# Optimization experiments

Measured on AMD Instinct MI355X. Metric: run time of the kernel, lower is better.

## Reference

```python
import jax, jax.numpy as jnp
import numpy as np

KS = 3            # kernel_size
DILS = (1, 2, 4)  # dilation_list == padding_list
EPS = 1e-5        # BN eps


def _unfold3(x, d):
    # emulate F.unfold(kernel=3, dilation=d, padding=d, stride=1).view(b, c, 9, h, w)
    b, c, h, w = x.shape
    xp = jnp.pad(x, ((0, 0), (0, 0), (d, d), (d, d)))
    pats = [xp[:, :, i * d:i * d + h, j * d:j * d + w] for i in range(KS) for j in range(KS)]
    return jnp.stack(pats, axis=2)


def _conv1x1(x, w, b):
    return jnp.einsum('bchw,oc->bohw', x, w) + b[None, :, None, None]


def _bn_relu(x, g, be, m, v):
    s = g / jnp.sqrt(v + EPS)
    return jax.nn.relu(x * s[None, :, None, None] + (be - m * s)[None, :, None, None])


def _proj(x, w1, b1, g1, be1, m1, v1, w2, b2, g2, be2, m2, v2):
    h = _bn_relu(_conv1x1(x, w1, b1), g1, be1, m1, v1)
    return _bn_relu(_conv1x1(h, w2, b2), g2, be2, m2, v2)


def setup_inputs():
    key = jax.random.key(0)
    Cin, Ck, Cv, Cout = 512, 256, 256, 512
    B, H, W = 4, 64, 64
    ks = iter(jax.random.split(key, 48))

    def nrm(shape, s=0.02):
        return jax.random.normal(next(ks), shape, jnp.float32) * s

    def bn(c):
        return (jnp.ones((c,), jnp.float32) + nrm((c,), 0.1),  # gamma
                nrm((c,), 0.1),                                 # beta
                nrm((c,), 0.1),                                 # running mean
                jax.random.uniform(next(ks), (c,), jnp.float32, 0.5, 1.5))  # running var

    inp = {"x": jax.random.normal(next(ks), (B, Cin, H, W), jnp.float32)}
    for p in ("k", "q"):
        g1, be1, m1, v1 = bn(Ck)
        g2, be2, m2, v2 = bn(Ck)
        inp.update({
            p + "1_w": nrm((Ck, Cin)), p + "1_b": nrm((Ck,)),
            p + "1_g": g1, p + "1_be": be1, p + "1_m": m1, p + "1_v": v1,
            p + "2_w": nrm((Ck, Ck)), p + "2_b": nrm((Ck,)),
            p + "2_g": g2, p + "2_be": be2, p + "2_m": m2, p + "2_v": v2,
        })
    inp["v_w"] = nrm((Cv, Cin)); inp["v_b"] = nrm((Cv,))
    inp["w_w"] = nrm((Cout, Cv)); inp["w_b"] = nrm((Cout,))
    return inp


def reference(x,
              k1_w, k1_b, k1_g, k1_be, k1_m, k1_v,
              k2_w, k2_b, k2_g, k2_be, k2_m, k2_v,
              q1_w, q1_b, q1_g, q1_be, q1_m, q1_v,
              q2_w, q2_b, q2_g, q2_be, q2_m, q2_v,
              v_w, v_b, w_w, w_b):
    # scale == 1: MaxPool2d(1x1-equivalent) and final bilinear resize are identities.
    value = _conv1x1(x, v_w, v_b)                                  # (b,cv,h,w)
    keyf = _proj(x, k1_w, k1_b, k1_g, k1_be, k1_m, k1_v,
                 k2_w, k2_b, k2_g, k2_be, k2_m, k2_v)              # (b,ck,h,w)
    query = _proj(x, q1_w, q1_b, q1_g, q1_be, q1_m, q1_v,
                  q2_w, q2_b, q2_g, q2_be, q2_m, q2_v)             # (b,ck,h,w)
    uk = jnp.concatenate([_unfold3(keyf, d) for d in DILS], axis=2)   # (b,ck,27,h,w)
    uv = jnp.concatenate([_unfold3(value, d) for d in DILS], axis=2)  # (b,cv,27,h,w)
    sim = jnp.sum(uk * query[:, :, None], axis=1, keepdims=True)      # (b,1,27,h,w)
    sim = jax.nn.softmax(sim, axis=2)
    context = jnp.sum(sim * uv, axis=2)                               # (b,cv,h,w)
    return _conv1x1(context, w_w, w_b)
```

## Files before the change

### kernel.cpp

```cpp
#include <hip/hip_runtime.h>

#define HW   4096
#define Hh   64
#define Ww   64
#define NB   27
#define EPSBN 1e-5f

typedef _Float16 f16x8 __attribute__((ext_vector_type(8)));
typedef _Float16 f16x4 __attribute__((ext_vector_type(4)));
typedef _Float16 f16x2 __attribute__((ext_vector_type(2)));
typedef float    f32x4 __attribute__((ext_vector_type(4)));

__device__ __forceinline__ void gld_lds16(const void* g, void* l) {
    __builtin_amdgcn_global_load_lds(
        (const __attribute__((address_space(1))) unsigned int*)g,
        (__attribute__((address_space(3))) unsigned int*)l, 16, 0, 0);
}

__global__ __launch_bounds__(256)
void prep_kernel(const float* s0, const float* s1, const float* s2,
                 const float* s3, const float* s4, const float* s5,
                 _Float16* d0, _Float16* d1, _Float16* d2,
                 _Float16* d3, _Float16* d4, _Float16* d5)
{
    const int bid = blockIdx.x;
    const int j  = bid >> 6;
    const int bx = bid & 63;
    const float* s = j==0?s0: j==1?s1: j==2?s2: j==3?s3: j==4?s4: s5;
    _Float16*  d = j==0?d0: j==1?d1: j==2?d2: j==3?d3: j==4?d4: d5;
    const int  n = (j==3 || j==4) ? 65536 : 131072;
    const int  i = (bx * 256 + threadIdx.x) * 8;
    if (i < n) {
        f16x8 h;
        #pragma unroll
        for (int k = 0; k < 8; ++k) h[k] = (_Float16)s[i + k];
        *(f16x8*)(d + i) = h;
    }
}

struct GJob {
    const _Float16* in;
    const float*    xf;
    const _Float16* w;
    const float* b; const float* g; const float* be; const float* m; const float* v;
    _Float16* oh;
    float*    of;
};

__global__ __launch_bounds__(512)
void gemm_f(GJob J0, GJob J1, GJob J2, int stage, int K, int JO, int mode)
{
    __shared__ _Float16 As[3 * 64 * 64];
    __shared__ _Float16 Bs[128 * 64];

    const int tid  = threadIdx.x;
    const int lane = tid & 63;
    const int w8   = tid >> 6;
    const int lr   = lane & 15;
    const int lg   = lane >> 4;
    const int wm   = w8 & 3;
    const int wn   = w8 >> 2;

    const int bid = blockIdx.x;
    const int xcd = bid & 7;
    const int jj  = bid >> 3;
    const int nb  = xcd * 16 + (jj >> 2);
    const int u   = jj & 3;

    const int nA = (stage == 1) ? 3 : 2;
    int js0, js1, js2, ob0, ob1, ob2;
    if (stage == 1)      { js0 = 0; js1 = 1; js2 = 2; ob0 = ob1 = ob2 = u * 64; }
    else if (stage == 2) { js0 = js1 = js2 = (u >> 1); ob0 = (u & 1) * 128; ob1 = ob0 + 64; ob2 = ob1; }
    else                 { js0 = js1 = js2 = 0; ob0 = u * 128; ob1 = ob0 + 64; ob2 = ob1; }

#define JSEL(js, f) ((js) == 0 ? J0.f : ((js) == 1 ? J1.f : J2.f))
    const _Float16* w0 = JSEL(js0, w);
    const _Float16* w1 = JSEL(js1, w);
    const _Float16* w2 = JSEL(js2, w);
    const float* b0 = JSEL(js0, b); const float* g0 = JSEL(js0, g);
    const float* be0 = JSEL(js0, be); const float* m0 = JSEL(js0, m); const float* v0 = JSEL(js0, v);
    const float* b1 = JSEL(js1, b); const float* g1 = JSEL(js1, g);
    const float* be1 = JSEL(js1, be); const float* m1 = JSEL(js1, m); const float* v1 = JSEL(js1, v);
    const float* b2 = JSEL(js2, b); const float* g2 = JSEL(js2, g);
    const float* be2 = JSEL(js2, be); const float* m2 = JSEL(js2, m); const float* v2 = JSEL(js2, v);
    _Float16* oh0 = JSEL(js0, oh); float* of0 = JSEL(js0, of);
    _Float16* oh1 = JSEL(js1, oh); float* of1 = JSEL(js1, of);
    _Float16* oh2 = JSEL(js2, oh); float* of2 = JSEL(js2, of);
    const _Float16* bIn = JSEL(js0, in);
    const float*    bXf = JSEL(js0, xf);
#undef JSEL

    const int scol = (((lane & 7) ^ (lane >> 3)) << 3);
    const int rowA = w8 * 8 + (lane >> 3);
    const _Float16* aS0 = w0 + (size_t)(ob0 + rowA) * K + scol;
    const _Float16* aS1 = w1 + (size_t)(ob1 + rowA) * K + scol;
    const _Float16* aS2 = w2 + (size_t)(ob2 + rowA) * K + scol;

    const int rowB = w8 * 16 + (lane >> 3);
    const _Float16* bS = bIn ? (bIn + (size_t)(nb * 128 + rowB) * K + scol) : nullptr;

    const int xrow  = tid & 127;
    const int chq   = tid >> 7;
    const int pgS   = nb * 128 + xrow;
    const float* xbase = bXf ? (bXf + ((size_t)(pgS >> 12) * 512) * HW + (pgS & 4095)) : nullptr;
    const int bxorw = (xrow & 7) << 4;
    const bool f32B = (bXf != nullptr);

    float fr[16];
    auto ISSUE_BX = [&](int rd) {
        const int cb = rd * 64 + chq * 16;
        #pragma unroll
        for (int i2 = 0; i2 < 16; ++i2)
            fr[i2] = xbase[(size_t)(cb + i2) * HW];
    };
    auto WRITE_BX = [&]() {
        #pragma unroll
        for (int g4 = 0; g4 < 2; ++g4) {
            f16x8 hv;
            #pragma unroll
            for (int i2 = 0; i2 < 8; ++i2) hv[i2] = (_Float16)fr[g4 * 8 + i2];
            *(f16x8*)((char*)Bs + xrow * 128 + ((chq * 32 + g4 * 16) ^ bxorw)) = hv;
        }
    };

    f32x4 acc0[4] = {}, acc1[4] = {}, acc2[4] = {};
    const int nr = K >> 6;

    if (f32B) ISSUE_BX(0);

    for (int rd = 0; rd < nr; ++rd) {
        const int kb = rd * 64;
        __syncthreads();
        if (f32B) {
            WRITE_BX();
        } else {
            gld_lds16(bS + kb,                 (char*)Bs + w8 * 2048);
            gld_lds16(bS + (size_t)8 * K + kb, (char*)Bs + w8 * 2048 + 1024);
        }
        gld_lds16(aS0 + kb, (char*)As + w8 * 1024);
        gld_lds16(aS1 + kb, (char*)As + 8192 + w8 * 1024);
        if (nA > 2) gld_lds16(aS2 + kb, (char*)As + 16384 + w8 * 1024);
        __syncthreads();
        if (f32B && rd + 1 < nr) ISSUE_BX(rd + 1);

        #pragma unroll
        for (int ks = 0; ks < 2; ++ks) {
            const int colx = (ks * 64 + lg * 16) ^ ((lr & 7) << 4);
            const int arow = (wm * 16 + lr) * 128 + colx;
            f16x8 bfr[4];
            #pragma unroll
            for (int t = 0; t < 4; ++t)
                bfr[t] = *(const f16x8*)((const char*)Bs + (wn * 64 + t * 16 + lr) * 128 + colx);
            const f16x8 af0 = *(const f16x8*)((const char*)As + arow);
            const f16x8 af1 = *(const f16x8*)((const char*)As + 8192 + arow);
            #pragma unroll
            for (int bj = 0; bj < 4; ++bj)
                acc0[bj] = __builtin_amdgcn_mfma_f32_16x16x32_f16(af0, bfr[bj], acc0[bj], 0, 0, 0);
            #pragma unroll
            for (int bj = 0; bj < 4; ++bj)
                acc1[bj] = __builtin_amdgcn_mfma_f32_16x16x32_f16(af1, bfr[bj], acc1[bj], 0, 0, 0);
            if (nA > 2) {
                const f16x8 af2 = *(const f16x8*)((const char*)As + 16384 + arow);
                #pragma unroll
                for (int bj = 0; bj < 4; ++bj)
                    acc2[bj] = __builtin_amdgcn_mfma_f32_16x16x32_f16(af2, bfr[bj], acc2[bj], 0, 0, 0);
            }
        }
    }

#define EPI(accS, obS, bS_, gS, beS, mS, vS, ohS, ofS) do {                      \
        const int o4 = (obS) + wm * 16 + lg * 4;                                 \
        float sc[4], off[4];                                                     \
        _Pragma("unroll")                                                        \
        for (int r = 0; r < 4; ++r) {                                            \
            const int o = o4 + r;                                                \
            if (gS) { float s = (gS)[o] * rsqrtf((vS)[o] + EPSBN);               \
                      sc[r] = s; off[r] = fmaf((bS_)[o] - (mS)[o], s, (beS)[o]); }\
            else    { sc[r] = 1.f; off[r] = (bS_)[o]; }                          \
        }                                                                        \
        _Pragma("unroll")                                                        \
        for (int bj = 0; bj < 4; ++bj) {                                         \
            const int pg = nb * 128 + wn * 64 + bj * 16 + lr;                    \
            float vv[4];                                                         \
            _Pragma("unroll")                                                    \
            for (int r = 0; r < 4; ++r) {                                        \
                float t = fmaf(accS[bj][r], sc[r], off[r]);                      \
                vv[r] = (gS) ? fmaxf(t, 0.f) : t;                                \
            }                                                                    \
            if (mode == 0) {                                                     \
                f16x4 hh;                                                        \
                _Pragma("unroll")                                                \
                for (int r = 0; r < 4; ++r) hh[r] = (_Float16)vv[r];             \
                *(f16x4*)((ohS) + (size_t)pg * JO + o4) = hh;                    \
            } else {                                                             \
                _Pragma("unroll")                                                \
                for (int r = 0; r < 4; ++r)                                      \
                    (ofS)[((size_t)(pg >> 12) * JO + o4 + r) * HW + (pg & 4095)] = vv[r]; \
            }                                                                    \
        }                                                                        \
    } while (0)

    EPI(acc0, ob0, b0, g0, be0, m0, v0, oh0, of0);
    EPI(acc1, ob1, b1, g1, be1, m1, v1, oh1, of1);
    if (nA > 2) EPI(acc2, ob2, b2, g2, be2, m2, v2, oh2, of2);
#undef EPI
}

__global__ __launch_bounds__(256)
void attn_fused(const _Float16* __restrict__ keyT, const _Float16* __restrict__ qryT,
                const _Float16* __restrict__ valT, _Float16* __restrict__ ctxT)
{
    const int tid  = threadIdx.x;
    const int slot = tid & 31;
    const int b    = blockIdx.y;
    const int p    = blockIdx.x * 8 + (tid >> 5);
    const int y    = p >> 6;
    const int xc   = p & 63;

    int   idx[NB];
    float valf[NB];
    #pragma unroll
    for (int n = 0; n < NB; ++n) {
        const int d  = (n < 9) ? 1 : (n < 18 ? 2 : 4);
        const int i  = (n / 3) % 3 - 1;
        const int j  = n % 3 - 1;
        const int yy = y + i * d, xx = xc + j * d;
        const bool ok = ((unsigned)yy < (unsigned)Hh) && ((unsigned)xx < (unsigned)Ww);
        idx[n]  = min(max(yy, 0), Hh - 1) * Ww + min(max(xx, 0), Ww - 1);
        valf[n] = ok ? 1.f : 0.f;
    }

    const size_t base = (size_t)b * HW * 256 + slot * 8;
    const f16x8 q8 = *(const f16x8*)(qryT + base + (size_t)p * 256);

    f16x2 qp[4];
    qp[0] = __builtin_shufflevector(q8, q8, 0, 1);
    qp[1] = __builtin_shufflevector(q8, q8, 2, 3);
    qp[2] = __builtin_shufflevector(q8, q8, 4, 5);
    qp[3] = __builtin_shufflevector(q8, q8, 6, 7);

    float sim[NB];
    #pragma unroll
    for (int n = 0; n < NB; ++n) {
        const f16x8 k8 = *(const f16x8*)(keyT + base + (size_t)idx[n] * 256);
        float s = 0.f;
        s = __builtin_amdgcn_fdot2(__builtin_shufflevector(k8, k8, 0, 1), qp[0], s, false);
        s = __builtin_amdgcn_fdot2(__builtin_shufflevector(k8, k8, 2, 3), qp[1], s, false);
        s = __builtin_amdgcn_fdot2(__builtin_shufflevector(k8, k8, 4, 5), qp[2], s, false);
        s = __builtin_amdgcn_fdot2(__builtin_shufflevector(k8, k8, 6, 7), qp[3], s, false);
        sim[n] = s;
    }

    #pragma unroll
    for (int n = 0; n < NB; ++n) {
        float s = sim[n];
        s += __shfl_xor(s, 1);
        s += __shfl_xor(s, 2);
        s += __shfl_xor(s, 4);
        s += __shfl_xor(s, 8);
        s += __shfl_xor(s, 16);
        sim[n] = s * valf[n];
    }

    float mx = sim[0];
    #pragma unroll
    for (int n = 1; n < NB; ++n) mx = fmaxf(mx, sim[n]);
    float sum = 0.f;
    #pragma unroll
    for (int n = 0; n < NB; ++n) { sim[n] = __expf(sim[n] - mx); sum += sim[n]; }
    const float inv = 1.f / sum;
    #pragma unroll
    for (int n = 0; n < NB; ++n) sim[n] = sim[n] * inv * valf[n];

    float acc[8];
    #pragma unroll
    for (int i = 0; i < 8; ++i) acc[i] = 0.f;
    #pragma unroll
    for (int n = 0; n < NB; ++n) {
        const f16x8 v8 = *(const f16x8*)(valT + base + (size_t)idx[n] * 256);
        const float w = sim[n];
        #pragma unroll
        for (int i = 0; i < 8; ++i) acc[i] = fmaf(w, (float)v8[i], acc[i]);
    }

    f16x8 h;
    #pragma unroll
    for (int i = 0; i < 8; ++i) h[i] = (_Float16)acc[i];
    *(f16x8*)(ctxT + base + (size_t)p * 256) = h;
}

extern "C" void kernel_launch(void* const* d_in, const int* in_sizes, int n_in,
                              void* d_out, int out_size, void* d_ws, size_t ws_size,
                              hipStream_t stream)
{
    (void)in_sizes; (void)n_in; (void)out_size; (void)ws_size;
    const float* x     = (const float*)d_in[0];
    const float* k1_w  = (const float*)d_in[1];
    const float* k1_b  = (const float*)d_in[2];
    const float* k1_g  = (const float*)d_in[3];
    const float* k1_be = (const float*)d_in[4];
    const float* k1_m  = (const float*)d_in[5];
    const float* k1_v  = (const float*)d_in[6];
    const float* k2_w  = (const float*)d_in[7];
    const float* k2_b  = (const float*)d_in[8];
    const float* k2_g  = (const float*)d_in[9];
    const float* k2_be = (const float*)d_in[10];
    const float* k2_m  = (const float*)d_in[11];
    const float* k2_v  = (const float*)d_in[12];
    const float* q1_w  = (const float*)d_in[13];
    const float* q1_b  = (const float*)d_in[14];
    const float* q1_g  = (const float*)d_in[15];
    const float* q1_be = (const float*)d_in[16];
    const float* q1_m  = (const float*)d_in[17];
    const float* q1_v  = (const float*)d_in[18];
    const float* q2_w  = (const float*)d_in[19];
    const float* q2_b  = (const float*)d_in[20];
    const float* q2_g  = (const float*)d_in[21];
    const float* q2_be = (const float*)d_in[22];
    const float* q2_m  = (const float*)d_in[23];
    const float* q2_v  = (const float*)d_in[24];
    const float* v_w   = (const float*)d_in[25];
    const float* v_b   = (const float*)d_in[26];
    const float* w_w   = (const float*)d_in[27];
    const float* w_b   = (const float*)d_in[28];

    _Float16* hw = (_Float16*)d_ws;
    const size_t SH = (size_t)4 * HW * 256;
    _Float16* wv_h  = hw;
    _Float16* wk1_h = wv_h  + 131072;
    _Float16* wq1_h = wk1_h + 131072;
    _Float16* wk2_h = wq1_h + 131072;
    _Float16* wq2_h = wk2_h + 65536;
    _Float16* ww_h  = wq2_h + 65536;
    _Float16* k1T   = ww_h  + 131072;
    _Float16* q1T   = k1T + SH;
    _Float16* valT  = q1T + SH;
    _Float16* ctxT  = valT + SH;
    _Float16* keyPC = ctxT + SH;
    _Float16* qryPC = keyPC + SH;

    prep_kernel<<<384, 256, 0, stream>>>(v_w, k1_w, q1_w, k2_w, q2_w, w_w,
                                         wv_h, wk1_h, wq1_h, wk2_h, wq2_h, ww_h);

    GJob jv  = { nullptr, x, wv_h,  v_b,  nullptr, nullptr, nullptr, nullptr, valT,  nullptr };
    GJob jk1 = { nullptr, x, wk1_h, k1_b, k1_g, k1_be, k1_m, k1_v,            k1T,   nullptr };
    GJob jq1 = { nullptr, x, wq1_h, q1_b, q1_g, q1_be, q1_m, q1_v,            q1T,   nullptr };
    GJob jk2 = { k1T, nullptr, wk2_h, k2_b, k2_g, k2_be, k2_m, k2_v,          keyPC, nullptr };
    GJob jq2 = { q1T, nullptr, wq2_h, q2_b, q2_g, q2_be, q2_m, q2_v,          qryPC, nullptr };
    GJob jw  = { ctxT, nullptr, ww_h, w_b,  nullptr, nullptr, nullptr, nullptr, nullptr, (float*)d_out };

    gemm_f<<<512, 512, 0, stream>>>(jv, jk1, jq1, 1, 512, 256, 0);
    gemm_f<<<512, 512, 0, stream>>>(jk2, jq2, jq2, 2, 256, 256, 0);
    attn_fused<<<dim3(512, 4), 256, 0, stream>>>(keyPC, qryPC, valT, ctxT);
    gemm_f<<<512, 512, 0, stream>>>(jw, jw, jw, 4, 256, 512, 2);
}
```

Before: 86.91 us.

## Halve GEMM block tile, double-buffer B in LDS, load A directly to registers

The 1x1-conv GEMM kernel now uses 256-thread blocks with a 64-pixel N tile instead of 128, launched as 1024 blocks. B tiles are double-buffered in LDS so the next K-slice is loaded during the current MFMA work, leaving one barrier per iteration. Weight (A) fragments are read straight from global memory into registers, so the A LDS staging is gone. The aim is more blocks, more latency hiding and less LDS traffic. The cost is that each block reuses less B data and issues uncoalesced, repeated global reads of the weights.

Result: slower. 115.1 us (+32.5%).

```diff
diff --git a/kernel.cpp b/kernel.cpp
--- a/kernel.cpp
+++ b/kernel.cpp
@@ -47,24 +47,21 @@
     float*    of;
 };
 
-__global__ __launch_bounds__(512)
+__global__ __launch_bounds__(256)
 void gemm_f(GJob J0, GJob J1, GJob J2, int stage, int K, int JO, int mode)
 {
-    __shared__ _Float16 As[3 * 64 * 64];
-    __shared__ _Float16 Bs[128 * 64];
+    __shared__ _Float16 Bs[2][64 * 64];
 
     const int tid  = threadIdx.x;
     const int lane = tid & 63;
-    const int w8   = tid >> 6;
+    const int w4   = tid >> 6;
     const int lr   = lane & 15;
     const int lg   = lane >> 4;
-    const int wm   = w8 & 3;
-    const int wn   = w8 >> 2;
 
     const int bid = blockIdx.x;
     const int xcd = bid & 7;
     const int jj  = bid >> 3;
-    const int nb  = xcd * 16 + (jj >> 2);
+    const int nb  = xcd * 32 + (jj >> 2);
     const int u   = jj & 3;
 
     const int nA = (stage == 1) ? 3 : 2;
@@ -90,18 +87,18 @@
     const float*    bXf = JSEL(js0, xf);
 #undef JSEL
 
+    const int arow = w4 * 16 + lr;
+    const _Float16* aP0 = w0 + (size_t)(ob0 + arow) * K + lg * 8;
+    const _Float16* aP1 = w1 + (size_t)(ob1 + arow) * K + lg * 8;
+    const _Float16* aP2 = w2 + (size_t)(ob2 + arow) * K + lg * 8;
+
     const int scol = (((lane & 7) ^ (lane >> 3)) << 3);
-    const int rowA = w8 * 8 + (lane >> 3);
-    const _Float16* aS0 = w0 + (size_t)(ob0 + rowA) * K + scol;
-    const _Float16* aS1 = w1 + (size_t)(ob1 + rowA) * K + scol;
-    const _Float16* aS2 = w2 + (size_t)(ob2 + rowA) * K + scol;
-
-    const int rowB = w8 * 16 + (lane >> 3);
-    const _Float16* bS = bIn ? (bIn + (size_t)(nb * 128 + rowB) * K + scol) : nullptr;
-
-    const int xrow  = tid & 127;
-    const int chq   = tid >> 7;
-    const int pgS   = nb * 128 + xrow;
+    const int rowB = w4 * 16 + (lane >> 3);
+    const _Float16* bS = bIn ? (bIn + (size_t)(nb * 64 + rowB) * K + scol) : nullptr;
+
+    const int xrow = tid & 63;
+    const int chq  = tid >> 6;
+    const int pgS  = nb * 64 + xrow;
     const float* xbase = bXf ? (bXf + ((size_t)(pgS >> 12) * 512) * HW + (pgS & 4095)) : nullptr;
     const int bxorw = (xrow & 7) << 4;
     const bool f32B = (bXf != nullptr);
@@ -113,46 +110,57 @@
         for (int i2 = 0; i2 < 16; ++i2)
             fr[i2] = xbase[(size_t)(cb + i2) * HW];
     };
-    auto WRITE_BX = [&]() {
+    auto WRITE_BX = [&](int buf) {
         #pragma unroll
         for (int g4 = 0; g4 < 2; ++g4) {
             f16x8 hv;
             #pragma unroll
             for (int i2 = 0; i2 < 8; ++i2) hv[i2] = (_Float16)fr[g4 * 8 + i2];
-            *(f16x8*)((char*)Bs + xrow * 128 + ((chq * 32 + g4 * 16) ^ bxorw)) = hv;
+            *(f16x8*)((char*)&Bs[buf][0] + xrow * 128 + ((chq * 32 + g4 * 16) ^ bxorw)) = hv;
         }
     };
+    auto GLD_B = [&](int rd, int buf) {
+        const int kb = rd * 64;
+        gld_lds16(bS + kb,                 (char*)&Bs[buf][0] + w4 * 2048);
+        gld_lds16(bS + (size_t)8 * K + kb, (char*)&Bs[buf][0] + w4 * 2048 + 1024);
+    };
 
     f32x4 acc0[4] = {}, acc1[4] = {}, acc2[4] = {};
     const int nr = K >> 6;
 
-    if (f32B) ISSUE_BX(0);
-
+    if (f32B) { ISSUE_BX(0); WRITE_BX(0); }
+    else      { GLD_B(0, 0); }
+    __syncthreads();
+
+    int cur = 0;
     for (int rd = 0; rd < nr; ++rd) {
+        const bool more = (rd + 1 < nr);
         const int kb = rd * 64;
-        __syncthreads();
-        if (f32B) {
-            WRITE_BX();
-        } else {
-            gld_lds16(bS + kb,                 (char*)Bs + w8 * 2048);
-            gld_lds16(bS + (size_t)8 * K + kb, (char*)Bs + w8 * 2048 + 1024);
+
+        f16x8 a00 = *(const f16x8*)(aP0 + kb);
+        f16x8 a01 = *(const f16x8*)(aP0 + kb + 32);
+        f16x8 a10 = *(const f16x8*)(aP1 + kb);
+        f16x8 a11 = *(const f16x8*)(aP1 + kb + 32);
+        f16x8 a20, a21;
+        if (nA > 2) {
+            a20 = *(const f16x8*)(aP2 + kb);
+            a21 = *(const f16x8*)(aP2 + kb + 32);
         }
-        gld_lds16(aS0 + kb, (char*)As + w8 * 1024);
-        gld_lds16(aS1 + kb, (char*)As + 8192 + w8 * 1024);
-        if (nA > 2) gld_lds16(aS2 + kb, (char*)As + 16384 + w8 * 1024);
-        __syncthreads();
-        if (f32B && rd + 1 < nr) ISSUE_BX(rd + 1);
+
+        if (more) {
+            if (f32B) ISSUE_BX(rd + 1);
+            else      GLD_B(rd + 1, cur ^ 1);
+        }
 
         #pragma unroll
         for (int ks = 0; ks < 2; ++ks) {
             const int colx = (ks * 64 + lg * 16) ^ ((lr & 7) << 4);
-            const int arow = (wm * 16 + lr) * 128 + colx;
             f16x8 bfr[4];
             #pragma unroll
             for (int t = 0; t < 4; ++t)
-                bfr[t] = *(const f16x8*)((const char*)Bs + (wn * 64 + t * 16 + lr) * 128 + colx);
-            const f16x8 af0 = *(const f16x8*)((const char*)As + arow);
-            const f16x8 af1 = *(const f16x8*)((const char*)As + 8192 + arow);
+                bfr[t] = *(const f16x8*)((const char*)&Bs[cur][0] + (t * 16 + lr) * 128 + colx);
+            const f16x8 af0 = ks ? a01 : a00;
+            const f16x8 af1 = ks ? a11 : a10;
             #pragma unroll
             for (int bj = 0; bj < 4; ++bj)
                 acc0[bj] = __builtin_amdgcn_mfma_f32_16x16x32_f16(af0, bfr[bj], acc0[bj], 0, 0, 0);
@@ -160,16 +168,20 @@
             for (int bj = 0; bj < 4; ++bj)
                 acc1[bj] = __builtin_amdgcn_mfma_f32_16x16x32_f16(af1, bfr[bj], acc1[bj], 0, 0, 0);
             if (nA > 2) {
-                const f16x8 af2 = *(const f16x8*)((const char*)As + 16384 + arow);
+                const f16x8 af2 = ks ? a21 : a20;
                 #pragma unroll
                 for (int bj = 0; bj < 4; ++bj)
                     acc2[bj] = __builtin_amdgcn_mfma_f32_16x16x32_f16(af2, bfr[bj], acc2[bj], 0, 0, 0);
             }
         }
+
+        if (f32B && more) WRITE_BX(cur ^ 1);
+        __syncthreads();
+        cur ^= 1;
     }
 
 #define EPI(accS, obS, bS_, gS, beS, mS, vS, ohS, ofS) do {                      \
-        const int o4 = (obS) + wm * 16 + lg * 4;                                 \
+        const int o4 = (obS) + w4 * 16 + lg * 4;                                 \
         float sc[4], off[4];                                                     \
         _Pragma("unroll")                                                        \
         for (int r = 0; r < 4; ++r) {                                            \
@@ -180,7 +192,7 @@
         }                                                                        \
         _Pragma("unroll")                                                        \
         for (int bj = 0; bj < 4; ++bj) {                                         \
-            const int pg = nb * 128 + wn * 64 + bj * 16 + lr;                    \
+            const int pg = nb * 64 + bj * 16 + lr;                               \
             float vv[4];                                                         \
             _Pragma("unroll")                                                    \
             for (int r = 0; r < 4; ++r) {                                        \
@@ -349,8 +361,8 @@
     GJob jq2 = { q1T, nullptr, wq2_h, q2_b, q2_g, q2_be, q2_m, q2_v,          qryPC, nullptr };
     GJob jw  = { ctxT, nullptr, ww_h, w_b,  nullptr, nullptr, nullptr, nullptr, nullptr, (float*)d_out };
 
-    gemm_f<<<512, 512, 0, stream>>>(jv, jk1, jq1, 1, 512, 256, 0);
-    gemm_f<<<512, 512, 0, stream>>>(jk2, jq2, jq2, 2, 256, 256, 0);
+    gemm_f<<<1024, 256, 0, stream>>>(jv, jk1, jq1, 1, 512, 256, 0);
+    gemm_f<<<1024, 256, 0, stream>>>(jk2, jq2, jq2, 2, 256, 256, 0);
     attn_fused<<<dim3(512, 4), 256, 0, stream>>>(keyPC, qryPC, valT, ctxT);
-    gemm_f<<<512, 512, 0, stream>>>(jw, jw, jw, 4, 256, 512, 2);
-}
+    gemm_f<<<1024, 256, 0, stream>>>(jw, jw, jw, 4, 256, 512, 2);
+}
```
